# Kernel optimization log

Measured on AMD Instinct MI355X. Metric: run time of the kernel, lower is better.

Reference implementation:

```python
import jax, jax.numpy as jnp
import numpy as np

TEMPERATURE = 34.0
PAD = 1  # kernel_size // 2

def setup_inputs() -> dict:
    key = jax.random.key(0)
    ks = jax.random.split(key, 5)
    B, C, H, W = 32, 256, 56, 56
    K, O, I, kh = 4, 256, 256, 3
    hidden = int(C * 0.25) + 1  # 65
    return {
        "x": jax.random.normal(ks[0], (B, C, H, W), jnp.float32),
        "fc1_w": jax.random.normal(ks[1], (hidden, C), jnp.float32) * (2.0 / C) ** 0.5,
        "fc2_w": jax.random.normal(ks[2], (K, hidden), jnp.float32) * (2.0 / hidden) ** 0.5,
        "fc2_b": jnp.zeros((K,), jnp.float32),
        "weight": jax.random.normal(ks[3], (K, O, I, kh, kh), jnp.float32) * (2.0 / (I * kh * kh)) ** 0.5,
        "bias": jnp.zeros((K, O), jnp.float32),
    }

def reference(x, fc1_w, fc2_w, fc2_b, weight, bias):
    # attention2d: global avg pool -> 1x1 conv (fc1) -> relu -> 1x1 conv (fc2) -> softmax(logits/T)
    pooled = x.mean(axis=(2, 3))                      # [B, C]
    h = jax.nn.relu(pooled @ fc1_w.T)                 # [B, hidden]
    logits = h @ fc2_w.T + fc2_b                      # [B, K]
    att = jax.nn.softmax(logits / TEMPERATURE, axis=1)
    # aggregate per-sample conv weights/bias over K kernel banks
    agg_w = jnp.einsum('bk,koihw->boihw', att, weight)  # [B, O, I, kh, kw]
    agg_b = att @ bias                                  # [B, O]
    # per-sample conv (torch emulates via groups=B): vmap over batch
    def conv_one(xi, wi):
        return jax.lax.conv_general_dilated(
            xi[None], wi, window_strides=(1, 1),
            padding=((PAD, PAD), (PAD, PAD)),
            dimension_numbers=('NCHW', 'OIHW', 'NCHW'))[0]
    out = jax.vmap(conv_one)(x, agg_w)                 # [B, O, H, W]
    return out + agg_b[:, :, None, None]
```

## Files before the change

### kernel.cpp

```cpp
#include <hip/hip_runtime.h>


typedef short bf16x8 __attribute__((ext_vector_type(8)));
typedef float f32x16 __attribute__((ext_vector_type(16)));

__device__ __forceinline__ unsigned short f2bf(float f) {
  unsigned int u = __float_as_uint(f);
  return (unsigned short)((u + 0x7FFFu + ((u >> 16) & 1u)) >> 16);
}
__device__ __forceinline__ float bf2f(unsigned short h) {
  return __uint_as_float(((unsigned int)h) << 16);
}

__device__ __forceinline__ int invswz(int S) {
  int b7 = (S >> 7) & 1;
  int b6 = ((S >> 6) & 1) ^ b7;
  int b5 = ((S >> 5) & 1) ^ b6;
  int b4 = ((S >> 4) & 1) ^ b5;
  return (S & ~0x70) | (b4 << 4) | (b5 << 5) | (b6 << 6);
}

typedef const __attribute__((address_space(1))) unsigned int* gas_t;
typedef __attribute__((address_space(3))) unsigned int* las_t;
__device__ __forceinline__ void dma16(const void* g, unsigned lds_addr) {
  __builtin_amdgcn_global_load_lds((gas_t)g, (las_t)(size_t)lds_addr, 16, 0, 0);
}

__global__ void xcast_k(const float* __restrict__ x, unsigned short* __restrict__ xb,
                        float* __restrict__ pooled) {
  __shared__ unsigned short tile[64 * 260];
  int b = blockIdx.y;
  int hw0 = blockIdx.x * 64;
  int t = threadIdx.x;
  int p = t & 15, g = t >> 4;
#pragma unroll
  for (int i = 0; i < 16; ++i) {
    int c = g + 16 * i;
    float4 v = *(const float4*)(x + ((size_t)(b * 256 + c)) * 3136 + hw0 + p * 4);
    tile[(p * 4 + 0) * 260 + c] = f2bf(v.x);
    tile[(p * 4 + 1) * 260 + c] = f2bf(v.y);
    tile[(p * 4 + 2) * 260 + c] = f2bf(v.z);
    tile[(p * 4 + 3) * 260 + c] = f2bf(v.w);
  }
  __syncthreads();
  int lane = t & 63, wq = t >> 6;
  int c4 = lane * 4;
#pragma unroll
  for (int it = 0; it < 16; ++it) {
    int hl = it * 4 + wq;
    ushort4 v = *(const ushort4*)&tile[hl * 260 + c4];
    *(ushort4*)&xb[((size_t)(b * 3136 + hw0 + hl)) * 256 + c4] = v;
  }
  float s = 0.f;
#pragma unroll 16
  for (int hl = 0; hl < 64; ++hl) s += bf2f(tile[hl * 260 + t]);
  atomicAdd(&pooled[b * 256 + t], s * (1.0f / 3136.0f));
}

__global__ void att_k(const float* __restrict__ pooled, const float* __restrict__ fc1,
                      const float* __restrict__ fc2w, const float* __restrict__ fc2b,
                      const float* __restrict__ bias, float* __restrict__ att,
                      float* __restrict__ aggb) {
  int b = blockIdx.x, t = threadIdx.x;
  __shared__ float p[256];
  __shared__ float h[65];
  __shared__ float a4[4];
  for (int i = t; i < 256; i += 64) p[i] = pooled[b * 256 + i];
  __syncthreads();
  for (int j = t; j < 65; j += 64) {
    float s = 0.f;
    for (int c = 0; c < 256; ++c) s += p[c] * fc1[j * 256 + c];
    h[j] = fmaxf(s, 0.f);
  }
  __syncthreads();
  if (t == 0) {
    float lg[4];
    for (int k = 0; k < 4; ++k) {
      float s = fc2b[k];
      for (int j = 0; j < 65; ++j) s += h[j] * fc2w[k * 65 + j];
      lg[k] = s * (1.0f / 34.0f);
    }
    float m = fmaxf(fmaxf(lg[0], lg[1]), fmaxf(lg[2], lg[3]));
    float e0 = expf(lg[0] - m), e1 = expf(lg[1] - m), e2 = expf(lg[2] - m), e3 = expf(lg[3] - m);
    float inv = 1.0f / (e0 + e1 + e2 + e3);
    a4[0] = e0 * inv; a4[1] = e1 * inv; a4[2] = e2 * inv; a4[3] = e3 * inv;
    for (int k = 0; k < 4; ++k) att[b * 4 + k] = a4[k];
  }
  __syncthreads();
  for (int o = t; o < 256; o += 64) {
    float s = 0.f;
    for (int k = 0; k < 4; ++k) s += a4[k] * bias[k * 256 + o];
    aggb[b * 256 + o] = s;
  }
}

__global__ void aggw_k(const float* __restrict__ weight, const float* __restrict__ att,
                       unsigned short* __restrict__ aggw) {
  __shared__ float wl[4 * 2304];
  int o = blockIdx.x, t = threadIdx.x;
  for (int k = 0; k < 4; ++k)
    for (int idx = t; idx < 2304; idx += 256)
      wl[k * 2304 + idx] = weight[((size_t)(k * 256 + o)) * 2304 + idx];
  __syncthreads();
  int ot = o >> 7, ol = o & 127, ic = t >> 4, il = t & 15;
  int b0 = blockIdx.y * 8;
  for (int b = b0; b < b0 + 8; ++b) {
    float a0 = att[b * 4 + 0], a1 = att[b * 4 + 1], a2 = att[b * 4 + 2], a3 = att[b * 4 + 3];
    size_t base = ((size_t)((b * 2 + ot) * 16 + ic)) * (9 * 2048) + ol * 16 + il;
#pragma unroll
    for (int r = 0; r < 9; ++r) {
      float s = a0 * wl[t * 9 + r] + a1 * wl[2304 + t * 9 + r] +
                a2 * wl[4608 + t * 9 + r] + a3 * wl[6912 + t * 9 + r];
      aggw[base + r * 2048] = f2bf(s);
    }
  }
}

#define XBUF 12288

__global__ __launch_bounds__(256, 3) void conv_k(const unsigned short* __restrict__ xb,
                                                 const unsigned short* __restrict__ aggw,
                                                 const float* __restrict__ aggb,
                                                 const float* __restrict__ zerobuf,
                                                 float* __restrict__ out) {
  __shared__ __align__(16) unsigned char lds[2 * XBUF];
  const unsigned ldsbase = (unsigned)(size_t)&lds[0];
  const int t = threadIdx.x;
  const int wid = t >> 6, lane = t & 63, l31 = lane & 31, q = lane >> 5;
  const int wo = wid >> 1, wn = wid & 1;

  int id = blockIdx.x;
  int wgid = (id & 7) * 200 + (id >> 3);
  int bn = wgid % 25;
  int rest = wgid / 25;
  int b = rest >> 1, bo = rest & 1;

  const int o0 = bo * 128;
  const int n0 = bn * 128;
  const int h0 = n0 / 56;

  int bbase[2], nn[2], swz[2][3];
#pragma unroll
  for (int nf = 0; nf < 2; ++nf) {
    int n = n0 + wn * 64 + nf * 32 + l31;
    int h = n / 56, w = n - h * 56;
    nn[nf] = n;
    bbase[nf] = ((h - h0) * 64 + w) * 32 + q * 16;
#pragma unroll
    for (int dw = 0; dw < 3; ++dw) swz[nf][dw] = ((w + dw) & 7) << 4;
  }
  int aoff[2];
#pragma unroll
  for (int mf = 0; mf < 2; ++mf) aoff[mf] = (wo * 64 + mf * 32 + l31) * 32 + q * 16;

  const char* xb_b = (const char*)xb + (size_t)b * 3136 * 512;
  const char* ag_c = (const char*)aggw + (size_t)rest * 589824;

  const char* xg[3];
#pragma unroll
  for (int j = 0; j < 3; ++j) {
    int S = (j * 256 + t) * 16;
    int L = invswz(S);
    int pos = L >> 5, sub = (L >> 4) & 1;
    int row = pos >> 6, col = pos & 63;
    int hg = h0 - 1 + row, wg = col - 1;
    bool valid = (col >= 1 && col <= 56 && hg >= 0 && hg < 56);
    xg[j] = valid ? (xb_b + (size_t)(hg * 56 + wg) * 512 + sub * 16) : (const char*)zerobuf;
  }

  f32x16 acc[2][2];
#pragma unroll
  for (int i = 0; i < 2; ++i)
#pragma unroll
    for (int j = 0; j < 2; ++j)
#pragma unroll
      for (int e = 0; e < 16; ++e) acc[i][j][e] = 0.f;

#pragma unroll
  for (int j = 0; j < 3; ++j) dma16(xg[j], ldsbase + j * 4096 + wid * 1024);
  __syncthreads();

  int cur = 0;
  for (int ic = 0; ic < 16; ++ic) {
    if (ic + 1 < 16) {
#pragma unroll
      for (int j = 0; j < 3; ++j)
        dma16(xg[j] + (ic + 1) * 32, ldsbase + (cur ^ 1) * XBUF + j * 4096 + wid * 1024);
      __builtin_amdgcn_sched_barrier(0);
    }
    const char* agc = ag_c + (size_t)ic * 36864;
    const unsigned char* xlds = lds + cur * XBUF;
    bf16x8 a0s[2], a1s[2];
    a0s[0] = *(const bf16x8*)(agc + aoff[0]);
    a1s[0] = *(const bf16x8*)(agc + aoff[1]);
    a0s[1] = *(const bf16x8*)(agc + 4096 + aoff[0]);
    a1s[1] = *(const bf16x8*)(agc + 4096 + aoff[1]);
#pragma unroll
    for (int r = 0; r < 9; ++r) {
      const int dh = r / 3, dw = r % 3;
      bf16x8 c0 = a0s[r & 1], c1 = a1s[r & 1];
      if (r + 2 < 9) {
        a0s[r & 1] = *(const bf16x8*)(agc + (r + 2) * 4096 + aoff[0]);
        a1s[r & 1] = *(const bf16x8*)(agc + (r + 2) * 4096 + aoff[1]);
      }
      bf16x8 b0 = *(const bf16x8*)(xlds + ((bbase[0] + dh * 2048 + dw * 32) ^ swz[0][dw]));
      bf16x8 b1 = *(const bf16x8*)(xlds + ((bbase[1] + dh * 2048 + dw * 32) ^ swz[1][dw]));
      __builtin_amdgcn_s_setprio(1);
      acc[0][0] = __builtin_amdgcn_mfma_f32_32x32x16_bf16(c0, b0, acc[0][0], 0, 0, 0);
      acc[0][1] = __builtin_amdgcn_mfma_f32_32x32x16_bf16(c0, b1, acc[0][1], 0, 0, 0);
      acc[1][0] = __builtin_amdgcn_mfma_f32_32x32x16_bf16(c1, b0, acc[1][0], 0, 0, 0);
      acc[1][1] = __builtin_amdgcn_mfma_f32_32x32x16_bf16(c1, b1, acc[1][1], 0, 0, 0);
      __builtin_amdgcn_s_setprio(0);
    }
    __syncthreads();
    cur ^= 1;
  }

#pragma unroll
  for (int mf = 0; mf < 2; ++mf) {
#pragma unroll
    for (int reg = 0; reg < 16; ++reg) {
      int o = o0 + wo * 64 + mf * 32 + (reg & 3) + 8 * (reg >> 2) + 4 * q;
      float ab = aggb[b * 256 + o];
      float* op = out + ((size_t)(b * 256 + o)) * 3136;
#pragma unroll
      for (int nf = 0; nf < 2; ++nf) {
        if (nn[nf] < 3136) op[nn[nf]] = acc[mf][nf][reg] + ab;
      }
    }
  }
}

extern "C" void kernel_launch(void* const* d_in, const int* in_sizes, int n_in,
                              void* d_out, int out_size, void* d_ws, size_t ws_size,
                              hipStream_t stream) {
  const float* x      = (const float*)d_in[0];
  const float* fc1    = (const float*)d_in[1];
  const float* fc2w   = (const float*)d_in[2];
  const float* fc2b   = (const float*)d_in[3];
  const float* weight = (const float*)d_in[4];
  const float* bias   = (const float*)d_in[5];
  float* out = (float*)d_out;

  char* ws = (char*)d_ws;
  float* pooled         = (float*)(ws);
  float* att            = (float*)(ws + 32768);
  float* aggb           = (float*)(ws + 33280);
  unsigned short* aggw  = (unsigned short*)(ws + 66048);
  unsigned short* xb    = (unsigned short*)(ws + 66048 + 37748736);

  hipMemsetAsync(pooled, 0, 32768, stream);
  xcast_k<<<dim3(49, 32), 256, 0, stream>>>(x, xb, pooled);
  att_k<<<32, 64, 0, stream>>>(pooled, fc1, fc2w, fc2b, bias, att, aggb);
  hipMemsetAsync(pooled, 0, 1024, stream);
  aggw_k<<<dim3(256, 4), 256, 0, stream>>>(weight, att, aggw);
  conv_k<<<1600, 256, 0, stream>>>(xb, aggw, aggb, (const float*)pooled, out);
}
```

Before: 226.1 us.

## Software-pipeline conv inner loop with register double-buffered A/B fragments

Restructures the per-input-channel-chunk loop into three phases of three filter taps each. A (weight) and B (LDS activation) fragments are double-buffered in registers, so the loads for the next phase are issued while the current phase's MFMAs run. The next chunk's first A fragments are prefetched before the barrier and its B fragments right after it, and the chunk loop is unrolled by two to alternate buffers. The extra registers this needs are made available by lowering launch bounds from 3 to 2 waves per SIMD, which trades occupancy for more in-flight loads per wave.

```diff
diff --git a/kernel.cpp b/kernel.cpp
--- a/kernel.cpp
+++ b/kernel.cpp
@@ -117,8 +117,60 @@
 }
 
 #define XBUF 12288
-
-__global__ __launch_bounds__(256, 3) void conv_k(const unsigned short* __restrict__ xb,
+#define MFMA32(a, b, c) __builtin_amdgcn_mfma_f32_32x32x16_bf16(a, b, c, 0, 0, 0)
+
+#define LOAD_A(S, base, t0)                                                    \
+  _Pragma("unroll") for (int j = 0; j < 3; ++j) {                              \
+    Ab[S][0][j] = *(const bf16x8*)((base) + ((t0) + j) * 4096 + aoff[0]);      \
+    Ab[S][1][j] = *(const bf16x8*)((base) + ((t0) + j) * 4096 + aoff[1]);      \
+  }
+
+#define LOAD_B(S, xs, t0)                                                      \
+  _Pragma("unroll") for (int j = 0; j < 3; ++j) {                              \
+    const int rr = (t0) + j, dh = rr / 3, dwq = rr % 3;                        \
+    Bb[S][0][j] = *(const bf16x8*)((xs) +                                      \
+        ((bbase[0] + dh * 2048 + dwq * 32) ^ swz[0][dwq]));                    \
+    Bb[S][1][j] = *(const bf16x8*)((xs) +                                      \
+        ((bbase[1] + dh * 2048 + dwq * 32) ^ swz[1][dwq]));                    \
+  }
+
+#define MFMA_PH(S)                                                             \
+  __builtin_amdgcn_s_setprio(1);                                               \
+  _Pragma("unroll") for (int j = 0; j < 3; ++j) {                              \
+    acc[0][0] = MFMA32(Ab[S][0][j], Bb[S][0][j], acc[0][0]);                   \
+    acc[0][1] = MFMA32(Ab[S][0][j], Bb[S][1][j], acc[0][1]);                   \
+    acc[1][0] = MFMA32(Ab[S][1][j], Bb[S][0][j], acc[1][0]);                   \
+    acc[1][1] = MFMA32(Ab[S][1][j], Bb[S][1][j], acc[1][1]);                   \
+  }                                                                            \
+  __builtin_amdgcn_s_setprio(0);
+
+#define CHUNK(P, ic)                                                           \
+  do {                                                                         \
+    const char* agc = ag_c + (size_t)(ic) * 36864;                             \
+    const unsigned char* xls = lds + (P) * XBUF;                               \
+    const bool more = (ic) + 1 < 16;                                           \
+             \
+    if (more) {                                                                \
+      _Pragma("unroll") for (int j = 0; j < 3; ++j)                            \
+        dma16(xg[j] + ((ic) + 1) * 32,                                         \
+              ldsbase + (1 - (P)) * XBUF + j * 4096 + wid * 1024);             \
+      __builtin_amdgcn_sched_barrier(0);                                       \
+    }                                                                          \
+    LOAD_A((P) ^ 1, agc, 3)                                                    \
+    LOAD_B((P) ^ 1, xls, 3)                                                    \
+    MFMA_PH(P)                                                                 \
+                                                                      \
+    LOAD_A(P, agc, 6)                                                          \
+    LOAD_B(P, xls, 6)                                                          \
+    MFMA_PH((P) ^ 1)                                                           \
+                           \
+    if (more) { LOAD_A((P) ^ 1, agc + 36864, 0) }                              \
+    MFMA_PH(P)                                                                 \
+    __syncthreads();     \
+    if (more) { LOAD_B((P) ^ 1, lds + (1 - (P)) * XBUF, 0) }                   \
+  } while (0)
+
+__global__ __launch_bounds__(256, 2) void conv_k(const unsigned short* __restrict__ xb,
                                                  const unsigned short* __restrict__ aggw,
                                                  const float* __restrict__ aggb,
                                                  const float* __restrict__ zerobuf,
@@ -176,44 +228,17 @@
 #pragma unroll
       for (int e = 0; e < 16; ++e) acc[i][j][e] = 0.f;
 
+  bf16x8 Ab[2][2][3], Bb[2][2][3];
+
 #pragma unroll
   for (int j = 0; j < 3; ++j) dma16(xg[j], ldsbase + j * 4096 + wid * 1024);
   __syncthreads();
-
-  int cur = 0;
-  for (int ic = 0; ic < 16; ++ic) {
-    if (ic + 1 < 16) {
-#pragma unroll
-      for (int j = 0; j < 3; ++j)
-        dma16(xg[j] + (ic + 1) * 32, ldsbase + (cur ^ 1) * XBUF + j * 4096 + wid * 1024);
-      __builtin_amdgcn_sched_barrier(0);
-    }
-    const char* agc = ag_c + (size_t)ic * 36864;
-    const unsigned char* xlds = lds + cur * XBUF;
-    bf16x8 a0s[2], a1s[2];
-    a0s[0] = *(const bf16x8*)(agc + aoff[0]);
-    a1s[0] = *(const bf16x8*)(agc + aoff[1]);
-    a0s[1] = *(const bf16x8*)(agc + 4096 + aoff[0]);
-    a1s[1] = *(const bf16x8*)(agc + 4096 + aoff[1]);
-#pragma unroll
-    for (int r = 0; r < 9; ++r) {
-      const int dh = r / 3, dw = r % 3;
-      bf16x8 c0 = a0s[r & 1], c1 = a1s[r & 1];
-      if (r + 2 < 9) {
-        a0s[r & 1] = *(const bf16x8*)(agc + (r + 2) * 4096 + aoff[0]);
-        a1s[r & 1] = *(const bf16x8*)(agc + (r + 2) * 4096 + aoff[1]);
-      }
-      bf16x8 b0 = *(const bf16x8*)(xlds + ((bbase[0] + dh * 2048 + dw * 32) ^ swz[0][dw]));
-      bf16x8 b1 = *(const bf16x8*)(xlds + ((bbase[1] + dh * 2048 + dw * 32) ^ swz[1][dw]));
-      __builtin_amdgcn_s_setprio(1);
-      acc[0][0] = __builtin_amdgcn_mfma_f32_32x32x16_bf16(c0, b0, acc[0][0], 0, 0, 0);
-      acc[0][1] = __builtin_amdgcn_mfma_f32_32x32x16_bf16(c0, b1, acc[0][1], 0, 0, 0);
-      acc[1][0] = __builtin_amdgcn_mfma_f32_32x32x16_bf16(c1, b0, acc[1][0], 0, 0, 0);
-      acc[1][1] = __builtin_amdgcn_mfma_f32_32x32x16_bf16(c1, b1, acc[1][1], 0, 0, 0);
-      __builtin_amdgcn_s_setprio(0);
-    }
-    __syncthreads();
-    cur ^= 1;
+  LOAD_A(0, ag_c, 0)
+  LOAD_B(0, lds, 0)
+
+  for (int icp = 0; icp < 8; ++icp) {
+    CHUNK(0, icp * 2);
+    CHUNK(1, icp * 2 + 1);
   }
 
 #pragma unroll
```

Result: slower. 239.6 us (+6.0%).
